# Optimization experiments

Hardware: AMD Instinct MI355X
Metric: run time of the kernel (lower is better)

The kernel has to match this reference:

```python
import jax, jax.numpy as jnp
import numpy as np

N_HEAD = 4
N_FEAT = 256
D_K = N_FEAT // N_HEAD
SCALE = 1.0  # self.scale (non-trainable, scale>0 and tr_scale=None)
INV_SQRT_DK = 1.0 / (D_K ** 0.5)


def sparsemax(z, scale=1.0):
    """Closed-form equivalent of the module's sort-based sparsemax loop.
    Projects onto the simplex of radius `scale`, then divides by scale.
    Matches the strict `>` support condition of the while-loop."""
    n = z.shape[-1]
    z_sorted = jnp.flip(jnp.sort(z, axis=-1), axis=-1)          # descending
    csum = jnp.cumsum(z_sorted, axis=-1)
    k = jnp.arange(1, n + 1, dtype=z.dtype)
    support = k * z_sorted > (csum - scale)                      # strict, as in torch loop
    k_max = jnp.sum(support, axis=-1, keepdims=True)             # int, >=1 in practice
    csum_k = jnp.take_along_axis(csum, k_max - 1, axis=-1)
    tau = (csum_k - scale) / k_max.astype(z.dtype)               # tau_z
    return jax.nn.relu(z - tau) / scale


def setup_inputs() -> dict:
    key = jax.random.key(0)
    ks = jax.random.split(key, 9)
    B, T1, T2 = 4, 2048, 2048
    query = jax.random.normal(ks[0], (B, T1, N_FEAT), jnp.float32)
    key_t = jax.random.normal(ks[1], (B, T2, N_FEAT), jnp.float32)
    value = jax.random.normal(ks[2], (B, T2, N_FEAT), jnp.float32)
    mask = jnp.ones((B, 1, T2), jnp.int32)
    s = 0.02
    Wq = jax.random.normal(ks[3], (N_FEAT, N_FEAT), jnp.float32) * s
    bq = jax.random.normal(ks[4], (N_FEAT,), jnp.float32) * s
    Wk = jax.random.normal(ks[5], (N_FEAT, N_FEAT), jnp.float32) * s
    bk = jax.random.normal(ks[6], (N_FEAT,), jnp.float32) * s
    Wv = jax.random.normal(ks[7], (N_FEAT, N_FEAT), jnp.float32) * s
    bv = jax.random.normal(ks[8], (N_FEAT,), jnp.float32) * s
    return {"query": query, "key": key_t, "value": value, "mask": mask,
            "Wq": Wq, "bq": bq, "Wk": Wk, "bk": bk, "Wv": Wv, "bv": bv}


def reference(query, key, value, mask, Wq, bq, Wk, bk, Wv, bv):
    B, T1, _ = query.shape
    # forward_qkv: project, split heads, L2-normalize q/k (cosine attention) * scale
    q = (query @ Wq.T + bq).reshape(B, T1, N_HEAD, D_K).transpose(0, 2, 1, 3)  # (B,H,T1,dk)
    k = (key @ Wk.T + bk).reshape(B, -1, N_HEAD, D_K).transpose(0, 2, 1, 3)    # (B,H,T2,dk)
    v = (value @ Wv.T + bv).reshape(B, -1, N_HEAD, D_K).transpose(0, 2, 1, 3)  # (B,H,T2,dk)
    q = q / jnp.linalg.norm(q, axis=-1, keepdims=True) * SCALE
    k = k / jnp.linalg.norm(k, axis=-1, keepdims=True) * SCALE
    scores = jnp.einsum('bhqd,bhkd->bhqk', q, k) * INV_SQRT_DK  # (B,H,T1,T2)
    # forward_attention with mask: fill masked with float min, sparsemax, zero masked
    m = (mask[:, None, :, :] == 0)                               # (B,1,1|T1,T2)
    min_val = jnp.finfo(scores.dtype).min
    scores = jnp.where(m, min_val, scores)
    attn = jnp.where(m, 0.0, sparsemax(scores, 1.0))
    x = jnp.einsum('bhqk,bhkd->bhqd', attn, v)
    x = x.transpose(0, 2, 1, 3).reshape(B, T1, N_HEAD * D_K)     # NOTE: linear_out is never applied in the original forward
    return attn, x
```

## Files before the change

kernel.cpp:

```cpp
#include <hip/hip_runtime.h>
#include <hip/hip_bf16.h>

#define NB 4
#define NH 4
#define TT 2048
#define DKK 64
#define NF 256
#define QT 16

typedef __attribute__((ext_vector_type(8))) short bf16x8;
typedef __attribute__((ext_vector_type(4))) short s16x4;
typedef __attribute__((ext_vector_type(4))) float f32x4;
typedef __hip_bfloat16 bf16;

__device__ __forceinline__ short f2bs(float f) {
    bf16 h = __float2bfloat16(f);
    return *reinterpret_cast<short*>(&h);
}
__device__ __forceinline__ float b2f(short s) {
    return __uint_as_float(((unsigned)(unsigned short)s) << 16);
}
__device__ __forceinline__ float wave_sum(float v) {
    #pragma unroll
    for (int off = 1; off < 64; off <<= 1) v += __shfl_xor(v, off);
    return v;
}
__device__ __forceinline__ void lds_barrier() {
    asm volatile("s_waitcnt lgkmcnt(0)" ::: "memory");
    __builtin_amdgcn_s_barrier();
    __builtin_amdgcn_sched_barrier(0);
}

__global__ __launch_bounds__(256)
void wcvt_kernel(const float* __restrict__ Wq, const float* __restrict__ Wk,
                 const float* __restrict__ Wv, const int* __restrict__ mask,
                 bf16* __restrict__ Wb, unsigned* __restrict__ mbits)
{
    if (blockIdx.x == 192) {
        int t = threadIdx.x;
        const int* mp = mask + t * 32;
        unsigned m = 0;
        #pragma unroll
        for (int j = 0; j < 32; ++j) m |= (mp[j] != 0 ? 1u : 0u) << j;
        mbits[t] = m;
        return;
    }
    int gid = (blockIdx.x * 256 + threadIdx.x) * 4;
    const float* src;
    int m = gid >> 16, off = gid & 65535;
    src = (m == 0) ? Wq : (m == 1) ? Wk : Wv;
    float4 v = *(const float4*)(src + off);
    s16x4 o = { f2bs(v.x), f2bs(v.y), f2bs(v.z), f2bs(v.w) };
    *(s16x4*)((short*)Wb + gid) = o;
}

__global__ __launch_bounds__(256, 4)
void qkv_kernel(const float* __restrict__ query, const float* __restrict__ key,
                const float* __restrict__ value, const bf16* __restrict__ Wb,
                const float* __restrict__ bq, const float* __restrict__ bk,
                const float* __restrict__ bv,
                bf16* __restrict__ qB, bf16* __restrict__ kA, bf16* __restrict__ vB)
{
    __shared__ char Xq[8192], Xk[8192], Xv[8192];
    __shared__ char bounce[24576];
    const int tid = threadIdx.x;
    const int bt0 = blockIdx.x * 16;
    const int b0 = bt0 >> 11, t0 = bt0 & (TT - 1);

    {
        int row = tid >> 4, c0 = (tid & 15) * 16;
        int swr = (row & 7) << 4;
        const float* qs = query + (size_t)(bt0 + row) * NF + c0;
        const float* ks = key   + (size_t)(bt0 + row) * NF + c0;
        const float* vs = value + (size_t)(bt0 + row) * NF + c0;
        #pragma unroll
        for (int j = 0; j < 4; ++j) {
            float4 a = *(const float4*)(qs + j * 4);
            float4 b = *(const float4*)(ks + j * 4);
            float4 c = *(const float4*)(vs + j * 4);
            int byt = (row * 512 + c0 * 2 + j * 8) ^ swr;
            *(s16x4*)(Xq + byt) = (s16x4){ f2bs(a.x), f2bs(a.y), f2bs(a.z), f2bs(a.w) };
            *(s16x4*)(Xk + byt) = (s16x4){ f2bs(b.x), f2bs(b.y), f2bs(b.z), f2bs(b.w) };
            *(s16x4*)(Xv + byt) = (s16x4){ f2bs(c.x), f2bs(c.y), f2bs(c.z), f2bs(c.w) };
        }
    }
    __syncthreads();

    const int lane = tid & 63;
    const int w = tid >> 6;
    const int l15 = lane & 15;
    const int g = lane >> 4;
    const int swl = (l15 & 7) << 4;

    f32x4 qa[4], ka[4], va[4];
    #pragma unroll
    for (int ct = 0; ct < 4; ++ct) {
        qa[ct] = (f32x4){0.f,0.f,0.f,0.f};
        ka[ct] = (f32x4){0.f,0.f,0.f,0.f};
        va[ct] = (f32x4){0.f,0.f,0.f,0.f};
    }
    const bf16* Wqb = Wb;
    const bf16* Wkb = Wb + 65536;
    const bf16* Wvb = Wb + 131072;

    #pragma unroll
    for (int kt = 0; kt < 8; ++kt) {
        int byt = (l15 * 512 + kt * 64 + g * 16) ^ swl;
        bf16x8 xq = *(const bf16x8*)(Xq + byt);
        bf16x8 xk = *(const bf16x8*)(Xk + byt);
        bf16x8 xv = *(const bf16x8*)(Xv + byt);
        #pragma unroll
        for (int ct = 0; ct < 4; ++ct) {
            size_t wo = (size_t)(w * 64 + ct * 16 + l15) * NF + kt * 32 + g * 8;
            bf16x8 aq = *(const bf16x8*)(Wqb + wo);
            bf16x8 ak = *(const bf16x8*)(Wkb + wo);
            bf16x8 av = *(const bf16x8*)(Wvb + wo);
            qa[ct] = __builtin_amdgcn_mfma_f32_16x16x32_bf16(aq, xq, qa[ct], 0, 0, 0);
            ka[ct] = __builtin_amdgcn_mfma_f32_16x16x32_bf16(ak, xk, ka[ct], 0, 0, 0);
            va[ct] = __builtin_amdgcn_mfma_f32_16x16x32_bf16(av, xv, va[ct], 0, 0, 0);
        }
    }

    float qv[4][4], kv[4][4], vv[4][4];
    float sq = 0.f, sk = 0.f;
    #pragma unroll
    for (int ct = 0; ct < 4; ++ct) {
        float4 b4q = *(const float4*)(bq + w * 64 + ct * 16 + g * 4);
        float4 b4k = *(const float4*)(bk + w * 64 + ct * 16 + g * 4);
        float4 b4v = *(const float4*)(bv + w * 64 + ct * 16 + g * 4);
        #pragma unroll
        for (int p = 0; p < 4; ++p) {
            float bqp = (p == 0) ? b4q.x : (p == 1) ? b4q.y : (p == 2) ? b4q.z : b4q.w;
            float bkp = (p == 0) ? b4k.x : (p == 1) ? b4k.y : (p == 2) ? b4k.z : b4k.w;
            float bvp = (p == 0) ? b4v.x : (p == 1) ? b4v.y : (p == 2) ? b4v.z : b4v.w;
            qv[ct][p] = qa[ct][p] + bqp;
            kv[ct][p] = ka[ct][p] + bkp;
            vv[ct][p] = va[ct][p] + bvp;
            sq = __builtin_fmaf(qv[ct][p], qv[ct][p], sq);
            sk = __builtin_fmaf(kv[ct][p], kv[ct][p], sk);
        }
    }
    sq += __shfl_xor(sq, 16); sq += __shfl_xor(sq, 32);
    sk += __shfl_xor(sk, 16); sk += __shfl_xor(sk, 32);
    float nq = rsqrtf(sq) * 0.125f;
    float nk = rsqrtf(sk);

    __syncthreads();
    #pragma unroll
    for (int ct = 0; ct < 4; ++ct) {
        int d5 = (ct & 1) * 16 + g * 4;
        int qb = w * 2048 + (ct >> 1) * 1024 + (d5 >> 3) * 256 + l15 * 16 + (d5 & 7) * 2;
        s16x4 oq = { f2bs(qv[ct][0]*nq), f2bs(qv[ct][1]*nq), f2bs(qv[ct][2]*nq), f2bs(qv[ct][3]*nq) };
        s16x4 ok = { f2bs(kv[ct][0]*nk), f2bs(kv[ct][1]*nk), f2bs(kv[ct][2]*nk), f2bs(kv[ct][3]*nk) };
        *(s16x4*)(bounce + qb)        = oq;
        *(s16x4*)(bounce + qb + 8192) = ok;
        #pragma unroll
        for (int p = 0; p < 4; ++p) {
            int vb = 16384 + w * 2048 + ct * 512 + (l15 >> 3) * 256 + (g * 4 + p) * 16 + (l15 & 7) * 2;
            *(short*)(bounce + vb) = f2bs(vv[ct][p]);
        }
    }
    __syncthreads();

    const int qt = t0 >> 4;
    const int kc = t0 >> 5, h16 = (t0 >> 4) & 1;
    for (int seg = tid; seg < 1536; seg += 256) {
        int byt = seg * 16;
        const char* src = bounce + byt;
        bf16* dst;
        if (byt < 8192) {
            int wh = byt >> 11, off = byt & 2047;
            dst = qB + (((size_t)(b0 * NH + wh)) * 128 + qt) * 1024 + off / 2;
        } else if (byt < 16384) {
            int r = byt - 8192;
            int wh = r >> 11, off = r & 2047;
            dst = kA + (((size_t)(b0 * NH + wh)) * 128 + qt) * 1024 + off / 2;
        } else {
            int r = byt - 16384;
            int wh = r >> 11, ct = (r >> 9) & 3, off = r & 511;
            dst = vB + ((((size_t)(b0 * NH + wh)) * 64 + kc) * 4 + ct) * 512 + h16 * 256 + off / 2;
        }
        *(bf16x8*)dst = *(const bf16x8*)src;
    }
}

__global__ __launch_bounds__(512, 4)
void attn_kernel(const bf16* __restrict__ qB, const bf16* __restrict__ kA,
                 const bf16* __restrict__ vB, const unsigned* __restrict__ mbits,
                 float* __restrict__ attn, float* __restrict__ xout)
{
    __shared__ short S_s[16 * 2048];
    __shared__ float4 xpart[4][64];
    const int tid = threadIdx.x;
    const int lane = tid & 63;
    const int w = tid >> 6;
    const int l15 = lane & 15;
    const int g = lane >> 4;
    const int swz = (blockIdx.x & 7) * 256 + (blockIdx.x >> 3);
    const int bh = swz >> 7;
    const int qt = swz & 127;
    const int q0 = qt * QT;
    const int b_ = bh >> 2, h_ = bh & 3;

    const size_t fb = (size_t)bh * 16384;
    const bf16x8* qBv = (const bf16x8*)qB + fb + (size_t)qt * 128;
    const bf16x8* kAv = (const bf16x8*)kA + fb;
    const bf16x8* vBv = (const bf16x8*)vB + fb;

    unsigned mreg[8];
    {
        const unsigned* mwp = mbits + b_ * 64 + w * 8;
        #pragma unroll
        for (int i = 0; i < 8; ++i) mreg[i] = mwp[i];
    }

    bf16x8 qf0 = qBv[lane];
    bf16x8 qf1 = qBv[64 + lane];

    f32x4 acc[16];
    #pragma unroll
    for (int t = 0; t < 16; ++t) acc[t] = (f32x4){0.f, 0.f, 0.f, 0.f};

    #pragma unroll
    for (int t = 0; t < 16; ++t) {
        int kt = w * 16 + t;
        bf16x8 kf0 = kAv[(kt * 2 + 0) * 64 + lane];
        bf16x8 kf1 = kAv[(kt * 2 + 1) * 64 + lane];
        acc[t] = __builtin_amdgcn_mfma_f32_16x16x32_bf16(kf0, qf0, acc[t], 0, 0, 0);
        acc[t] = __builtin_amdgcn_mfma_f32_16x16x32_bf16(kf1, qf1, acc[t], 0, 0, 0);
    }

    const short NEGB = (short)0xFF7F;
    char* prow = (char*)S_s + l15 * 4096;
    const int sw = (l15 & 7) << 4;
    #pragma unroll
    for (int t = 0; t < 16; ++t) {
        unsigned bits = mreg[t >> 1] >> (((t & 1) << 4) + (g << 2));
        s16x4 sb;
        sb[0] = (bits & 1) ? f2bs(acc[t][0]) : NEGB;
        sb[1] = (bits & 2) ? f2bs(acc[t][1]) : NEGB;
        sb[2] = (bits & 4) ? f2bs(acc[t][2]) : NEGB;
        sb[3] = (bits & 8) ? f2bs(acc[t][3]) : NEGB;
        *(s16x4*)(prow + ((w * 512 + t * 32 + g * 8) ^ sw)) = sb;
    }
    lds_barrier();

    const int r0 = 2 * w;
    float va[2][32];
    #pragma unroll
    for (int h = 0; h < 2; ++h) {
        const char* sr = (const char*)S_s + (r0 + h) * 4096;
        int swr = ((r0 + h) & 7) << 4;
        #pragma unroll
        for (int jj = 0; jj < 8; ++jj) {
            s16x4 p4 = *(const s16x4*)(sr + ((jj * 512 + lane * 8) ^ swr));
            va[h][jj * 4 + 0] = b2f(p4[0]);
            va[h][jj * 4 + 1] = b2f(p4[1]);
            va[h][jj * 4 + 2] = b2f(p4[2]);
            va[h][jj * 4 + 3] = b2f(p4[3]);
        }
    }

    #pragma unroll
    for (int h = 0; h < 2; ++h) {
        float S = 0.f, C = 0.f, Qs = 0.f;
        #pragma unroll
        for (int i = 0; i < 32; ++i) {
            float v = va[h][i];
            bool un = v > -1.0e30f;
            float sv = un ? v : 0.f;
            S += sv;
            C += un ? 1.f : 0.f;
            Qs = __builtin_fmaf(sv, sv, Qs);
        }
        S = wave_sum(S); C = wave_sum(C); Qs = wave_sum(Qs);
        float tu, prevC;
        bool done;
        if (C < 0.5f) { tu = 3.0e38f; done = true; prevC = 0.f; }
        else {
            float mu = S / C;
            float var = Qs / C - mu * mu;
            var = var > 0.f ? var : 0.f;
            tu = mu + 1.7f * __builtin_sqrtf(var);
            prevC = -1.f;
            done = false;
        }
        for (int it = 0; it < 64 && !done; ++it) {
            float S2 = 0.f, C2 = 0.f;
            #pragma unroll
            for (int i = 0; i < 32; ++i) {
                float v = va[h][i];
                bool in = v > tu;
                S2 += in ? v : 0.f;
                C2 += in ? 1.f : 0.f;
            }
            S2 = wave_sum(S2); C2 = wave_sum(C2);
            if (C2 == prevC) done = true;
            else if (C2 < 0.5f) { tu = (S - 1.f) / C; prevC = -1.f; }
            else { tu = (S2 - 1.f) / C2; prevC = C2; }
        }
        char* sr = (char*)S_s + (r0 + h) * 4096;
        int swr = ((r0 + h) & 7) << 4;
        float* ar = attn + ((size_t)bh * TT + q0 + r0 + h) * TT;
        #pragma unroll
        for (int jj = 0; jj < 8; ++jj) {
            f32x4 o;
            s16x4 pb4;
            #pragma unroll
            for (int e = 0; e < 4; ++e) {
                float a = va[h][jj * 4 + e] - tu;
                a = a > 0.f ? a : 0.f;
                o[e] = a;
                pb4[e] = f2bs(a);
            }
            __builtin_nontemporal_store(o, (f32x4*)(ar + jj * 256 + lane * 4));
            *(s16x4*)(sr + ((jj * 512 + lane * 8) ^ swr)) = pb4;
        }
    }
    lds_barrier();

    const int ds = w & 3;
    const int kh = w >> 2;
    f32x4 xacc = (f32x4){0.f, 0.f, 0.f, 0.f};
    __builtin_amdgcn_s_setprio(1);
    #pragma unroll 8
    for (int kcl = 0; kcl < 32; ++kcl) {
        int kc = kh * 32 + kcl;
        bf16x8 af = *(const bf16x8*)(prow + ((kh * 2048 + kcl * 64 + g * 16) ^ sw));
        bf16x8 bfr = vBv[(kc * 4 + ds) * 64 + lane];
        xacc = __builtin_amdgcn_mfma_f32_16x16x32_bf16(af, bfr, xacc, 0, 0, 0);
    }
    __builtin_amdgcn_s_setprio(0);
    if (w >= 4) xpart[w - 4][lane] = make_float4(xacc[0], xacc[1], xacc[2], xacc[3]);
    lds_barrier();
    if (w < 4) {
        float4 xp4 = xpart[w][lane];
        xacc[0] += xp4.x; xacc[1] += xp4.y; xacc[2] += xp4.z; xacc[3] += xp4.w;
        float* xp = xout + ((size_t)b_ * TT + q0 + g * 4) * NF + h_ * DKK + ds * 16 + l15;
        #pragma unroll
        for (int p = 0; p < 4; ++p)
            __builtin_nontemporal_store(xacc[p], xp + p * NF);
    }
}

extern "C" void kernel_launch(void* const* d_in, const int* in_sizes, int n_in,
                              void* d_out, int out_size, void* d_ws, size_t ws_size,
                              hipStream_t stream) {
    const float* query = (const float*)d_in[0];
    const float* key   = (const float*)d_in[1];
    const float* value = (const float*)d_in[2];
    const int*   mask  = (const int*)d_in[3];
    const float* Wq = (const float*)d_in[4];
    const float* bq = (const float*)d_in[5];
    const float* Wk = (const float*)d_in[6];
    const float* bk = (const float*)d_in[7];
    const float* Wv = (const float*)d_in[8];
    const float* bv = (const float*)d_in[9];

    float* attn = (float*)d_out;
    float* x    = (float*)d_out + (size_t)NB * NH * TT * TT;

    const size_t FRAG = (size_t)NB * NH * 16384 * 8;
    bf16* Wb = (bf16*)d_ws;
    bf16* qB = Wb + 3 * 65536;
    bf16* kA = qB + FRAG;
    bf16* vB = kA + FRAG;
    unsigned* mbits = (unsigned*)(vB + FRAG);

    wcvt_kernel<<<dim3(193), dim3(256), 0, stream>>>(Wq, Wk, Wv, mask, Wb, mbits);
    qkv_kernel<<<dim3(NB * TT / 16), dim3(256), 0, stream>>>(
        query, key, value, Wb, bq, bk, bv, qB, kA, vB);
    attn_kernel<<<dim3(NB * NH * (TT / QT)), dim3(512), 0, stream>>>(
        qB, kA, vB, mbits, attn, x);
}
```

Baseline: 127.4 us.

## Process 32 query rows per block with 1024 threads to reuse K/V fragments

Each attention block now handles two 16-row query tiles with 16 waves. The score phase reuses every loaded K fragment for both query tiles, and the PV phase reuses each V fragment across both row tiles, with 4 k-segments reduced through shared memory. The aim is to halve the global K/V fragment traffic per query row. In exchange, LDS per block doubles to 128KB for scores, which limits residency to one block per CU. The hidden middle section (sparsemax over rows) must also be adapted to 16 waves and 32 rows, and that part is not visible here.

```diff
diff --git a/kernel.cpp b/kernel.cpp
--- a/kernel.cpp
+++ b/kernel.cpp
@@ -6,7 +6,6 @@
 #define TT 2048
 #define DKK 64
 #define NF 256
-#define QT 16
 
 typedef __attribute__((ext_vector_type(8))) short bf16x8;
 typedef __attribute__((ext_vector_type(4))) short s16x4;
@@ -184,64 +183,76 @@
     }
 }
 
-__global__ __launch_bounds__(512, 4)
+__global__ __launch_bounds__(1024, 4)
 void attn_kernel(const bf16* __restrict__ qB, const bf16* __restrict__ kA,
                  const bf16* __restrict__ vB, const unsigned* __restrict__ mbits,
                  float* __restrict__ attn, float* __restrict__ xout)
 {
-    __shared__ short S_s[16 * 2048];
-    __shared__ float4 xpart[4][64];
+    __shared__ short S_s[32 * 2048];
+    __shared__ float4 xpart[3][4][2][64];
     const int tid = threadIdx.x;
     const int lane = tid & 63;
     const int w = tid >> 6;
     const int l15 = lane & 15;
     const int g = lane >> 4;
-    const int swz = (blockIdx.x & 7) * 256 + (blockIdx.x >> 3);
-    const int bh = swz >> 7;
-    const int qt = swz & 127;
-    const int q0 = qt * QT;
+    const int swz = (blockIdx.x & 7) * 128 + (blockIdx.x >> 3);
+    const int bh = swz >> 6;
+    const int qtb = swz & 63;
+    const int q0 = qtb * 32;
+    const int qt0 = qtb * 2;
     const int b_ = bh >> 2, h_ = bh & 3;
 
     const size_t fb = (size_t)bh * 16384;
-    const bf16x8* qBv = (const bf16x8*)qB + fb + (size_t)qt * 128;
+    const bf16x8* qBv = (const bf16x8*)qB + fb;
     const bf16x8* kAv = (const bf16x8*)kA + fb;
     const bf16x8* vBv = (const bf16x8*)vB + fb;
 
-    unsigned mreg[8];
+    unsigned mreg[4];
     {
-        const unsigned* mwp = mbits + b_ * 64 + w * 8;
-        #pragma unroll
-        for (int i = 0; i < 8; ++i) mreg[i] = mwp[i];
-    }
-
-    bf16x8 qf0 = qBv[lane];
-    bf16x8 qf1 = qBv[64 + lane];
-
-    f32x4 acc[16];
-    #pragma unroll
-    for (int t = 0; t < 16; ++t) acc[t] = (f32x4){0.f, 0.f, 0.f, 0.f};
-
-    #pragma unroll
-    for (int t = 0; t < 16; ++t) {
-        int kt = w * 16 + t;
+        const unsigned* mwp = mbits + b_ * 64 + w * 4;
+        #pragma unroll
+        for (int i = 0; i < 4; ++i) mreg[i] = mwp[i];
+    }
+
+    bf16x8 qf[2][2];
+    #pragma unroll
+    for (int qi = 0; qi < 2; ++qi) {
+        qf[qi][0] = qBv[(qt0 + qi) * 128 + lane];
+        qf[qi][1] = qBv[(qt0 + qi) * 128 + 64 + lane];
+    }
+
+    f32x4 acc[2][8];
+    #pragma unroll
+    for (int qi = 0; qi < 2; ++qi)
+        #pragma unroll
+        for (int t = 0; t < 8; ++t) acc[qi][t] = (f32x4){0.f, 0.f, 0.f, 0.f};
+
+    #pragma unroll
+    for (int t = 0; t < 8; ++t) {
+        int kt = w * 8 + t;
         bf16x8 kf0 = kAv[(kt * 2 + 0) * 64 + lane];
         bf16x8 kf1 = kAv[(kt * 2 + 1) * 64 + lane];
-        acc[t] = __builtin_amdgcn_mfma_f32_16x16x32_bf16(kf0, qf0, acc[t], 0, 0, 0);
-        acc[t] = __builtin_amdgcn_mfma_f32_16x16x32_bf16(kf1, qf1, acc[t], 0, 0, 0);
+        acc[0][t] = __builtin_amdgcn_mfma_f32_16x16x32_bf16(kf0, qf[0][0], acc[0][t], 0, 0, 0);
+        acc[0][t] = __builtin_amdgcn_mfma_f32_16x16x32_bf16(kf1, qf[0][1], acc[0][t], 0, 0, 0);
+        acc[1][t] = __builtin_amdgcn_mfma_f32_16x16x32_bf16(kf0, qf[1][0], acc[1][t], 0, 0, 0);
+        acc[1][t] = __builtin_amdgcn_mfma_f32_16x16x32_bf16(kf1, qf[1][1], acc[1][t], 0, 0, 0);
     }
 
     const short NEGB = (short)0xFF7F;
-    char* prow = (char*)S_s + l15 * 4096;
     const int sw = (l15 & 7) << 4;
     #pragma unroll
-    for (int t = 0; t < 16; ++t) {
-        unsigned bits = mreg[t >> 1] >> (((t & 1) << 4) + (g << 2));
-        s16x4 sb;
-        sb[0] = (bits & 1) ? f2bs(acc[t][0]) : NEGB;
-        sb[1] = (bits & 2) ? f2bs(acc[t][1]) : NEGB;
-        sb[2] = (bits & 4) ? f2bs(acc[t][2]) : NEGB;
-        sb[3] = (bits & 8) ? f2bs(acc[t][3]) : NEGB;
-        *(s16x4*)(prow + ((w * 512 + t * 32 + g * 8) ^ sw)) = sb;
+    for (int qi = 0; qi < 2; ++qi) {
+        char* prow = (char*)S_s + (qi * 16 + l15) * 4096;
+        #pragma unroll
+        for (int t = 0; t < 8; ++t) {
+            unsigned bits = mreg[t >> 1] >> (((t & 1) << 4) + (g << 2));
+            s16x4 sb;
+            sb[0] = (bits & 1) ? f2bs(acc[qi][t][0]) : NEGB;
+            sb[1] = (bits & 2) ? f2bs(acc[qi][t][1]) : NEGB;
+            sb[2] = (bits & 4) ? f2bs(acc[qi][t][2]) : NEGB;
+            sb[3] = (bits & 8) ? f2bs(acc[qi][t][3]) : NEGB;
+            *(s16x4*)(prow + ((w * 256 + t * 32 + g * 8) ^ sw)) = sb;
+        }
     }
     lds_barrier();
 
@@ -320,26 +331,43 @@
     lds_barrier();
 
     const int ds = w & 3;
-    const int kh = w >> 2;
-    f32x4 xacc = (f32x4){0.f, 0.f, 0.f, 0.f};
+    const int kseg = w >> 2;
+    f32x4 xacc[2];
+    xacc[0] = (f32x4){0.f, 0.f, 0.f, 0.f};
+    xacc[1] = (f32x4){0.f, 0.f, 0.f, 0.f};
     __builtin_amdgcn_s_setprio(1);
-    #pragma unroll 8
-    for (int kcl = 0; kcl < 32; ++kcl) {
-        int kc = kh * 32 + kcl;
-        bf16x8 af = *(const bf16x8*)(prow + ((kh * 2048 + kcl * 64 + g * 16) ^ sw));
+    #pragma unroll 4
+    for (int kcl = 0; kcl < 16; ++kcl) {
+        int kc = kseg * 16 + kcl;
         bf16x8 bfr = vBv[(kc * 4 + ds) * 64 + lane];
-        xacc = __builtin_amdgcn_mfma_f32_16x16x32_bf16(af, bfr, xacc, 0, 0, 0);
+        #pragma unroll
+        for (int rt = 0; rt < 2; ++rt) {
+            bf16x8 af = *(const bf16x8*)((char*)S_s + (rt * 16 + l15) * 4096
+                                         + ((kc * 64 + g * 16) ^ sw));
+            xacc[rt] = __builtin_amdgcn_mfma_f32_16x16x32_bf16(af, bfr, xacc[rt], 0, 0, 0);
+        }
     }
     __builtin_amdgcn_s_setprio(0);
-    if (w >= 4) xpart[w - 4][lane] = make_float4(xacc[0], xacc[1], xacc[2], xacc[3]);
+    if (kseg > 0) {
+        #pragma unroll
+        for (int rt = 0; rt < 2; ++rt)
+            xpart[kseg - 1][ds][rt][lane] = make_float4(xacc[rt][0], xacc[rt][1], xacc[rt][2], xacc[rt][3]);
+    }
     lds_barrier();
-    if (w < 4) {
-        float4 xp4 = xpart[w][lane];
-        xacc[0] += xp4.x; xacc[1] += xp4.y; xacc[2] += xp4.z; xacc[3] += xp4.w;
-        float* xp = xout + ((size_t)b_ * TT + q0 + g * 4) * NF + h_ * DKK + ds * 16 + l15;
-        #pragma unroll
-        for (int p = 0; p < 4; ++p)
-            __builtin_nontemporal_store(xacc[p], xp + p * NF);
+    if (kseg == 0) {
+        #pragma unroll
+        for (int rt = 0; rt < 2; ++rt) {
+            #pragma unroll
+            for (int s = 0; s < 3; ++s) {
+                float4 xp4 = xpart[s][ds][rt][lane];
+                xacc[rt][0] += xp4.x; xacc[rt][1] += xp4.y;
+                xacc[rt][2] += xp4.z; xacc[rt][3] += xp4.w;
+            }
+            float* xp = xout + ((size_t)b_ * TT + q0 + rt * 16 + g * 4) * NF + h_ * DKK + ds * 16 + l15;
+            #pragma unroll
+            for (int p = 0; p < 4; ++p)
+                __builtin_nontemporal_store(xacc[rt][p], xp + p * NF);
+        }
     }
 }
 
@@ -370,6 +398,6 @@
     wcvt_kernel<<<dim3(193), dim3(256), 0, stream>>>(Wq, Wk, Wv, mask, Wb, mbits);
     qkv_kernel<<<dim3(NB * TT / 16), dim3(256), 0, stream>>>(
         query, key, value, Wb, bq, bk, bv, qB, kA, vB);
-    attn_kernel<<<dim3(NB * NH * (TT / QT)), dim3(512), 0, stream>>>(
+    attn_kernel<<<dim3(NB * NH * (TT / 32)), dim3(1024), 0, stream>>>(
         qB, kA, vB, mbits, attn, x);
 }
```

After: 135.4 us. 6.3% more time.
